# Performance work log

Hardware: AMD Instinct MI355X
Metric: run time of the kernel (lower is better)

## Reference

```python
import jax, jax.numpy as jnp
import numpy as np

EMBED = 256; HEADS = 8; LEVELS = 4; POINTS = 4; HEAD_DIM = EMBED // HEADS
B = 2; Q = 20000; HP = 128; WP = 128
EPS = 1e-5


def setup_inputs() -> dict:
    key = jax.random.key(0)
    ks = jax.random.split(key, 12)
    s = 1.0 / np.sqrt(EMBED)
    return {
        "query": jax.random.normal(ks[0], (Q, EMBED), jnp.float32),
        "query_spatial_positions": jax.random.uniform(ks[1], (Q, 2), jnp.float32),
        "query_batch_offsets": jnp.array([0, Q // 2, Q], dtype=jnp.int32),
        "stacked_feature_maps": jax.random.normal(ks[2], (B, HP, WP, LEVELS, EMBED), jnp.float32),
        "level_spatial_shapes": jnp.array([[128, 128], [64, 64], [32, 32], [16, 16]], dtype=jnp.int32),
        "norm_gamma": jnp.ones((EMBED,), jnp.float32),
        "norm_beta": jnp.zeros((EMBED,), jnp.float32),
        "W_q": jax.random.normal(ks[3], (EMBED, EMBED), jnp.float32) * s,
        "W_off": jax.random.normal(ks[4], (EMBED, HEADS * LEVELS * POINTS * 2), jnp.float32) * s * 0.1,
        "b_off": jax.random.normal(ks[5], (HEADS * LEVELS * POINTS * 2,), jnp.float32) * 0.5,
        "W_attn": jax.random.normal(ks[6], (EMBED, HEADS * LEVELS * POINTS), jnp.float32) * s,
        "b_attn": jnp.zeros((HEADS * LEVELS * POINTS,), jnp.float32),
        "W_val": jax.random.normal(ks[7], (EMBED, EMBED), jnp.float32) * s,
        "b_val": jnp.zeros((EMBED,), jnp.float32),
        "W_out": jax.random.normal(ks[8], (EMBED, EMBED), jnp.float32) * s,
    }


def _layernorm(x, g, b):
    mu = x.mean(-1, keepdims=True)
    xc = x - mu
    v = (xc * xc).mean(-1, keepdims=True)
    return xc * jax.lax.rsqrt(v + EPS) * g + b


def reference(query, query_spatial_positions, query_batch_offsets, stacked_feature_maps,
              level_spatial_shapes, norm_gamma, norm_beta, W_q, W_off, b_off,
              W_attn, b_attn, W_val, b_val, W_out):
    residual = query
    x = _layernorm(query, norm_gamma, norm_beta)
    x = x @ W_q  # q_in_proj (no bias)

    off = (x @ W_off + b_off).reshape(Q, HEADS, LEVELS, POINTS, 2)
    attn = jax.nn.softmax((x @ W_attn + b_attn).reshape(Q, HEADS, LEVELS * POINTS), axis=-1)
    attn = attn.reshape(Q, HEADS, LEVELS, POINTS)

    # value projection over all levels, split into heads: [B,HP,WP,L,H,HD]
    value = (stacked_feature_maps @ W_val + b_val).reshape(B, HP, WP, LEVELS, HEADS, HEAD_DIM)

    shp = level_spatial_shapes.astype(jnp.float32)  # [L,2] (h,w)
    # normalized ref point + offset scaled by level size -> pixel coords (align_corners=False)
    loc = query_spatial_positions[:, None, None, None, :] + off / shp[None, None, :, None, :]
    pix = loc * shp[None, None, :, None, :] - 0.5  # [Q,H,L,P,2]
    py, px = pix[..., 0], pix[..., 1]
    y0 = jnp.floor(py); x0 = jnp.floor(px)
    wy = py - y0; wx = px - x0
    y0i = y0.astype(jnp.int32); x0i = x0.astype(jnp.int32)

    Hl = level_spatial_shapes[:, 0][None, None, :, None]
    Wl = level_spatial_shapes[:, 1][None, None, :, None]
    b_idx = (jnp.searchsorted(query_batch_offsets, jnp.arange(Q, dtype=jnp.int32), side='right') - 1)[:, None, None, None]
    l_idx = jnp.arange(LEVELS)[None, None, :, None]
    h_idx = jnp.arange(HEADS)[None, :, None, None]

    def gather(yi, xi, w):
        m = (yi >= 0) & (yi < Hl) & (xi >= 0) & (xi < Wl)  # zero-pad outside level extent
        yc = jnp.clip(yi, 0, HP - 1)
        xc = jnp.clip(xi, 0, WP - 1)
        v = value[b_idx, yc, xc, l_idx, h_idx]  # [Q,H,L,P,HD]
        return v * (w * m)[..., None]

    samp = (gather(y0i, x0i, (1 - wy) * (1 - wx))
            + gather(y0i, x0i + 1, (1 - wy) * wx)
            + gather(y0i + 1, x0i, wy * (1 - wx))
            + gather(y0i + 1, x0i + 1, wy * wx))

    out = (attn[..., None] * samp).sum(axis=(2, 3)).reshape(Q, EMBED)
    return out @ W_out + residual
```

## Files before the change

### kernel.cpp

```cpp
#include <hip/hip_runtime.h>
#include <hip/hip_bf16.h>
#include <stdint.h>

#define EMBED 256
#define HEADS 8
#define LEVELS 4
#define POINTS 4
#define HEAD_DIM 32
#define HPAD 128
#define WPAD 128
#define LN_EPS 1e-5f

typedef unsigned short u16;
typedef __attribute__((ext_vector_type(8))) short bf16x8v;
typedef __attribute__((ext_vector_type(4))) float f32x4;

static __device__ __forceinline__ float bu2f(u16 u) {
  return __uint_as_float(((unsigned)u) << 16);
}
static __device__ __forceinline__ u16 f2bu(float f) {
  unsigned x = __float_as_uint(f);
  return (u16)((x + 0x7fffu + ((x >> 16) & 1u)) >> 16);
}
static __device__ __forceinline__ float loadf(const void* p, size_t i, int isbf) {
  return isbf ? bu2f(((const u16*)p)[i]) : ((const float*)p)[i];
}
static __device__ __forceinline__ int imin(int a, int b) { return a < b ? a : b; }

static __device__ __forceinline__ void cp16(const u16* g, u16* l) {
  __builtin_amdgcn_global_load_lds((const __attribute__((address_space(1))) unsigned*)g,
                                   (__attribute__((address_space(3))) unsigned*)l, 16, 0, 0);
}

__global__ __launch_bounds__(256) void detect_kernel(const unsigned* __restrict__ q,
                                                     int* __restrict__ flag) {
  int t = threadIdx.x;
  __shared__ int s[256];
  unsigned u = q[t * 13 + 1];
  unsigned e = (u >> 7) & 0xFF;
  s[t] = (e >= 116 && e <= 130) ? 1 : 0;
  __syncthreads();
  for (int st = 128; st > 0; st >>= 1) { if (t < st) s[t] += s[t + st]; __syncthreads(); }
  if (t == 0) *flag = (s[0] > 200) ? 1 : 0;
}

__global__ __launch_bounds__(384) void boa_kernel(const void* __restrict__ b_off,
                                                  const void* __restrict__ b_attn,
                                                  float* __restrict__ boa,
                                                  const int* __restrict__ dflag) {
  int fl = *dflag;
  int t = threadIdx.x;
  boa[t] = (t < 256) ? loadf(b_off, t, fl) : loadf(b_attn, t - 256, fl);
}

__global__ __launch_bounds__(256) void wtrans_kernel(const void* __restrict__ W,
                                                     u16* __restrict__ Wt,
                                                     int K, int N,
                                                     const int* __restrict__ dflag) {
  int fl = *dflag;
  __shared__ float tile[32][33];
  int tx = threadIdx.x & 31, ty = threadIdx.x >> 5;
  int k0 = blockIdx.x * 32, n0 = blockIdx.y * 32;
#pragma unroll
  for (int j = 0; j < 4; j++) {
    int r = ty + j * 8;
    tile[r][tx] = loadf(W, (size_t)(k0 + r) * N + n0 + tx, fl);
  }
  __syncthreads();
#pragma unroll
  for (int j = 0; j < 4; j++) {
    int n = ty + j * 8;
    Wt[(size_t)(n0 + n) * K + k0 + tx] = f2bu(tile[tx][n]);
  }
}

__global__ __launch_bounds__(256) void ln_kernel(const void* __restrict__ q,
                                                 const void* __restrict__ g,
                                                 const void* __restrict__ be,
                                                 u16* __restrict__ out,
                                                 const int* __restrict__ dflag) {
  int fl = *dflag;
  int row = blockIdx.x;
  int t = threadIdx.x;
  __shared__ float sh[256];
  float v = loadf(q, (size_t)row * EMBED + t, fl);
  sh[t] = v;
  __syncthreads();
  for (int s = 128; s > 0; s >>= 1) { if (t < s) sh[t] += sh[t + s]; __syncthreads(); }
  float mu = sh[0] * (1.f / 256.f);
  __syncthreads();
  float xc = v - mu;
  sh[t] = xc * xc;
  __syncthreads();
  for (int s = 128; s > 0; s >>= 1) { if (t < s) sh[t] += sh[t + s]; __syncthreads(); }
  float r = rsqrtf(sh[0] * (1.f / 256.f) + LN_EPS);
  out[(size_t)row * EMBED + t] = f2bu(xc * r * loadf(g, t, fl) + loadf(be, t, fl));
}

template <int OUTMODE, bool ABF>
__global__ __launch_bounds__(256) void mfma_gemm(const void* __restrict__ A,
                                                 const u16* __restrict__ Bt,
                                                 const void* __restrict__ bias, int BiasC,
                                                 const void* __restrict__ resid,
                                                 void* __restrict__ Cv,
                                                 int M, int N, int K,
                                                 const int* __restrict__ dflag) {
  int fl = *dflag;
  __shared__ u16 As[4096];
  __shared__ u16 Bs[4096];
  int tid = threadIdx.x;
  int m0 = blockIdx.x * 128, n0 = blockIdx.y * 128;
  int wave = tid >> 6, lane = tid & 63;
  int quad = lane >> 4, r16 = lane & 15;
  int wm = (wave >> 1) * 64, wn = (wave & 1) * 64;

  f32x4 acc[4][4];
#pragma unroll
  for (int i = 0; i < 4; i++)
#pragma unroll
    for (int j = 0; j < 4; j++) acc[i][j] = (f32x4){0.f, 0.f, 0.f, 0.f};

  int p0 = tid, p1 = tid + 256;
  int r0 = p0 >> 2, c0 = (p0 & 3) * 8;
  int r1 = p1 >> 2, c1 = (p1 & 3) * 8;
  int ra0 = imin(m0 + r0, M - 1), ra1 = imin(m0 + r1, M - 1);

  const u16*   Ab = (const u16*)A;
  const float* Af = (const float*)A;

  for (int k0 = 0; k0 < K; k0 += 32) {
    __syncthreads();
    if (ABF) {
      cp16(Ab + (size_t)ra0 * K + k0 + c0, &As[p0 * 8]);
      cp16(Ab + (size_t)ra1 * K + k0 + c1, &As[p1 * 8]);
    } else if (fl) {
      *(int4*)&As[p0 * 8] = *(const int4*)(Ab + (size_t)ra0 * K + k0 + c0);
      *(int4*)&As[p1 * 8] = *(const int4*)(Ab + (size_t)ra1 * K + k0 + c1);
    } else {
      float4 f00 = *(const float4*)(Af + (size_t)ra0 * K + k0 + c0);
      float4 f01 = *(const float4*)(Af + (size_t)ra0 * K + k0 + c0 + 4);
      float4 f10 = *(const float4*)(Af + (size_t)ra1 * K + k0 + c1);
      float4 f11 = *(const float4*)(Af + (size_t)ra1 * K + k0 + c1 + 4);
      u16* d0 = &As[p0 * 8];
      d0[0] = f2bu(f00.x); d0[1] = f2bu(f00.y); d0[2] = f2bu(f00.z); d0[3] = f2bu(f00.w);
      d0[4] = f2bu(f01.x); d0[5] = f2bu(f01.y); d0[6] = f2bu(f01.z); d0[7] = f2bu(f01.w);
      u16* d1 = &As[p1 * 8];
      d1[0] = f2bu(f10.x); d1[1] = f2bu(f10.y); d1[2] = f2bu(f10.z); d1[3] = f2bu(f10.w);
      d1[4] = f2bu(f11.x); d1[5] = f2bu(f11.y); d1[6] = f2bu(f11.z); d1[7] = f2bu(f11.w);
    }
    cp16(Bt + (size_t)(n0 + r0) * K + k0 + c0, &Bs[p0 * 8]);
    cp16(Bt + (size_t)(n0 + r1) * K + k0 + c1, &Bs[p1 * 8]);
    __syncthreads();

    bf16x8v a[4], b[4];
#pragma unroll
    for (int i = 0; i < 4; i++)
      a[i] = *(const bf16x8v*)&As[(wm + i * 16 + r16) * 32 + quad * 8];
#pragma unroll
    for (int j = 0; j < 4; j++)
      b[j] = *(const bf16x8v*)&Bs[(wn + j * 16 + r16) * 32 + quad * 8];
#pragma unroll
    for (int i = 0; i < 4; i++)
#pragma unroll
      for (int j = 0; j < 4; j++)
        acc[i][j] = __builtin_amdgcn_mfma_f32_16x16x32_bf16(a[i], b[j], acc[i][j], 0, 0, 0);
  }

  int obf = (OUTMODE == 2) ? fl : OUTMODE;
  int bfl = (BiasC == 2) ? fl : 0;
  if (bias) {
#pragma unroll
    for (int j = 0; j < 4; j++) {
      float bv = loadf(bias, n0 + wn + j * 16 + r16, bfl);
#pragma unroll
      for (int i = 0; i < 4; i++)
#pragma unroll
        for (int reg = 0; reg < 4; reg++) acc[i][j][reg] += bv;
    }
  }

  if (obf) {
    int sl0 = (quad << 4) | ((2 * r16) & 15);
    int sl1 = sl0 + 1;
    bool lohalf = (r16 < 8);
#pragma unroll
    for (int i = 0; i < 4; i++) {
#pragma unroll
      for (int jp = 0; jp < 2; jp++) {
#pragma unroll
        for (int reg = 0; reg < 4; reg++) {
          float vA = acc[i][jp * 2][reg], vB = acc[i][jp * 2 + 1][reg];
          float a0 = __shfl(vA, sl0), a1 = __shfl(vA, sl1);
          float b0 = __shfl(vB, sl0), b1 = __shfl(vB, sl1);
          float lo = lohalf ? a0 : b0;
          float hi = lohalf ? a1 : b1;
          int row = m0 + wm + i * 16 + quad * 4 + reg;
          if (row < M) {
            size_t base = (size_t)row * N + n0 + wn + jp * 32 + 2 * r16;
            if (resid) {
              lo += loadf(resid, base, fl);
              hi += loadf(resid, base + 1, fl);
            }
            unsigned pk = (unsigned)f2bu(lo) | ((unsigned)f2bu(hi) << 16);
            *(unsigned*)((u16*)Cv + base) = pk;
          }
        }
      }
    }
  } else {
#pragma unroll
    for (int j = 0; j < 4; j++) {
      int col = n0 + wn + j * 16 + r16;
#pragma unroll
      for (int i = 0; i < 4; i++) {
#pragma unroll
        for (int reg = 0; reg < 4; reg++) {
          int row = m0 + wm + i * 16 + quad * 4 + reg;
          if (row < M) {
            float v = acc[i][j][reg];
            if (resid) v += loadf(resid, (size_t)row * N + col, fl);
            ((float*)Cv)[(size_t)row * N + col] = v;
          }
        }
      }
    }
  }
}

__global__ __launch_bounds__(512) void val_gemm(const void* __restrict__ A,
                                                const u16* __restrict__ Bt,
                                                const void* __restrict__ bias,
                                                u16* __restrict__ Cv,
                                                int M, const int* __restrict__ dflag) {
  int fl = *dflag;
  __shared__ u16 As[128 * 256];
  int tid = threadIdx.x;
  int m0 = blockIdx.x * 128;
  int wave = tid >> 6, lane = tid & 63;
  int quad = lane >> 4, r16 = lane & 15;
  int wm = (wave >> 2) * 64, wn = (wave & 3) * 64;

  if (fl) {
    const uint4* A16 = (const uint4*)A;
#pragma unroll
    for (int i = 0; i < 8; i++) {
      int g = i * 512 + tid;
      int r = g >> 5, c = g & 31;
      int rg = imin(m0 + r, M - 1);
      uint4 v = A16[(size_t)rg * 32 + c];
      *(uint4*)&As[r * 256 + ((c ^ (r & 7)) * 8)] = v;
    }
  } else {
    const float4* A4 = (const float4*)A;
#pragma unroll
    for (int p = 0; p < 2; p++) {
      float4 f[8];
#pragma unroll
      for (int q = 0; q < 8; q++) {
        int g = (p * 8 + q) * 512 + tid;
        int rg = imin(m0 + (g >> 6), M - 1);
        f[q] = A4[(size_t)rg * 64 + (g & 63)];
      }
#pragma unroll
      for (int q = 0; q < 8; q++) {
        int g = (p * 8 + q) * 512 + tid;
        int r = g >> 6, cw = g & 63;
        int c = cw >> 1, sub = cw & 1;
        uint2 w;
        w.x = (unsigned)f2bu(f[q].x) | ((unsigned)f2bu(f[q].y) << 16);
        w.y = (unsigned)f2bu(f[q].z) | ((unsigned)f2bu(f[q].w) << 16);
        *(uint2*)&As[r * 256 + ((c ^ (r & 7)) * 8) + sub * 4] = w;
      }
    }
  }
  __syncthreads();

  f32x4 acc[4][4];
#pragma unroll
  for (int i = 0; i < 4; i++)
#pragma unroll
    for (int j = 0; j < 4; j++) acc[i][j] = (f32x4){0.f, 0.f, 0.f, 0.f};

  int arow[4], arl[4];
#pragma unroll
  for (int i = 0; i < 4; i++) {
    arow[i] = (wm + i * 16 + r16) * 256;
    arl[i]  = (wm + i * 16 + r16) & 7;
  }
  const u16* bbase[4];
#pragma unroll
  for (int j = 0; j < 4; j++)
    bbase[j] = Bt + (size_t)(wn + j * 16 + r16) * 256 + quad * 8;

#pragma unroll
  for (int t = 0; t < 8; t++) {
    bf16x8v b[4];
#pragma unroll
    for (int j = 0; j < 4; j++)
      b[j] = *(const bf16x8v*)(bbase[j] + t * 32);
    bf16x8v a[4];
#pragma unroll
    for (int i = 0; i < 4; i++) {
      int chunk = ((t << 2) | quad) ^ arl[i];
      a[i] = *(const bf16x8v*)&As[arow[i] + chunk * 8];
    }
#pragma unroll
    for (int i = 0; i < 4; i++)
#pragma unroll
      for (int j = 0; j < 4; j++)
        acc[i][j] = __builtin_amdgcn_mfma_f32_16x16x32_bf16(a[i], b[j], acc[i][j], 0, 0, 0);
  }

#pragma unroll
  for (int j = 0; j < 4; j++) {
    float bv = loadf(bias, wn + j * 16 + r16, fl);
#pragma unroll
    for (int i = 0; i < 4; i++)
#pragma unroll
      for (int reg = 0; reg < 4; reg++) acc[i][j][reg] += bv;
  }
  int sl0 = (quad << 4) | ((2 * r16) & 15);
  int sl1 = sl0 + 1;
  bool lohalf = (r16 < 8);
#pragma unroll
  for (int i = 0; i < 4; i++) {
#pragma unroll
    for (int jp = 0; jp < 2; jp++) {
#pragma unroll
      for (int reg = 0; reg < 4; reg++) {
        float vA = acc[i][jp * 2][reg], vB = acc[i][jp * 2 + 1][reg];
        float a0 = __shfl(vA, sl0), a1 = __shfl(vA, sl1);
        float b0 = __shfl(vB, sl0), b1 = __shfl(vB, sl1);
        float lo = lohalf ? a0 : b0;
        float hi = lohalf ? a1 : b1;
        int row = m0 + wm + i * 16 + quad * 4 + reg;
        if (row < M) {
          size_t base = (size_t)row * 256 + wn + jp * 32 + 2 * r16;
          unsigned pk = (unsigned)f2bu(lo) | ((unsigned)f2bu(hi) << 16);
          *(unsigned*)(Cv + base) = pk;
        }
      }
    }
  }
}

__global__ __launch_bounds__(256) void sample2_kernel(const float* __restrict__ oa,
                                                      const void* __restrict__ qsp,
                                                      const int* __restrict__ qbo, int nb,
                                                      const int* __restrict__ lss,
                                                      const u16* __restrict__ value,
                                                      u16* __restrict__ samp, int Qn,
                                                      const int* __restrict__ dflag) {
  int fl = *dflag;
  int t = threadIdx.x;
  int q2 = t >> 7;
  int i7 = t & 127;
  int qb = blockIdx.x * 2;
  int q = imin(qb + q2, Qn - 1);

  __shared__ float Loff[2][256];
  __shared__ float Lw[2][128];
  __shared__ int   Lb[2];
  __shared__ int   Co[2][128][4];
  __shared__ float Cw[2][128][4];

  {
    const float* row = oa + (size_t)q * 384;
    float2 v = ((const float2*)row)[i7];
    Loff[q2][i7 * 2]     = v.x;
    Loff[q2][i7 * 2 + 1] = v.y;
    Lw[q2][i7] = row[256 + i7];
  }
  if (t < 2) {
    int qq = imin(qb + t, Qn - 1);
    int b = 0;
    for (int i = 1; i < nb; i++) if (qq >= qbo[i]) b = i;
    Lb[t] = b;
  }
  __syncthreads();

  if (t < 16) {
    int sq = t >> 3, h = t & 7;
    float* w = &Lw[sq][h * 16];
    float mx = w[0];
    for (int i = 1; i < 16; i++) mx = fmaxf(mx, w[i]);
    float s = 0.f;
    for (int i = 0; i < 16; i++) { float e = __expf(w[i] - mx); w[i] = e; s += e; }
    float inv = 1.f / s;
    for (int i = 0; i < 16; i++) w[i] *= inv;
  }
  __syncthreads();

  {
    int h = i7 >> 4, lp = i7 & 15, l = lp >> 2;
    int Hi = lss[l * 2], Wi = lss[l * 2 + 1];
    float Hl = (float)Hi, Wl = (float)Wi;
    float qy = loadf(qsp, (size_t)q * 2, fl);
    float qx = loadf(qsp, (size_t)q * 2 + 1, fl);
    float a  = Lw[q2][i7];
    float oy = Loff[q2][i7 * 2], ox = Loff[q2][i7 * 2 + 1];
    float py = (qy + oy / Hl) * Hl - 0.5f;
    float px = (qx + ox / Wl) * Wl - 0.5f;
    float y0f = floorf(py), x0f = floorf(px);
    float wy = py - y0f, wx = px - x0f;
    int y0 = (int)y0f, x0 = (int)x0f;
    int bbase = Lb[q2] * (HPAD * WPAD * LEVELS * EMBED);
#pragma unroll
    for (int c = 0; c < 4; c++) {
      int yi = y0 + (c >> 1), xi = x0 + (c & 1);
      float w = ((c >> 1) ? wy : 1.f - wy) * ((c & 1) ? wx : 1.f - wx);
      bool ok = (yi >= 0) & (yi < Hi) & (xi >= 0) & (xi < Wi);
      Co[q2][i7][c] = ok ? (bbase + ((yi * WPAD + xi) * LEVELS + l) * EMBED + h * HEAD_DIM) : 0;
      Cw[q2][i7][c] = ok ? (a * w) : 0.f;
    }
  }
  __syncthreads();

  {
    int h = (t >> 4) & 7;
    int d2 = t & 15;
    float ax = 0.f, ay = 0.f;
#pragma unroll
    for (int lp = 0; lp < 16; lp++) {
      int4   o4 = *(const int4*)&Co[q2][h * 16 + lp][0];
      float4 w4 = *(const float4*)&Cw[q2][h * 16 + lp][0];
      unsigned v;
      v = *(const unsigned*)(value + o4.x + d2 * 2);
      ax += w4.x * __uint_as_float(v << 16); ay += w4.x * __uint_as_float(v & 0xffff0000u);
      v = *(const unsigned*)(value + o4.y + d2 * 2);
      ax += w4.y * __uint_as_float(v << 16); ay += w4.y * __uint_as_float(v & 0xffff0000u);
      v = *(const unsigned*)(value + o4.z + d2 * 2);
      ax += w4.z * __uint_as_float(v << 16); ay += w4.z * __uint_as_float(v & 0xffff0000u);
      v = *(const unsigned*)(value + o4.w + d2 * 2);
      ax += w4.w * __uint_as_float(v << 16); ay += w4.w * __uint_as_float(v & 0xffff0000u);
    }
    if (qb + q2 < Qn) {
      unsigned pk = (unsigned)f2bu(ax) | ((unsigned)f2bu(ay) << 16);
      *(unsigned*)(samp + (size_t)(qb + q2) * 256 + h * 32 + d2 * 2) = pk;
    }
  }
}

extern "C" void kernel_launch(void* const* d_in, const int* in_sizes, int n_in,
                              void* d_out, int out_size, void* d_ws, size_t ws_size,
                              hipStream_t stream) {
  const void* query  = d_in[0];
  const void* qsp    = d_in[1];
  const int*  qbo    = (const int*)d_in[2];
  const void* sfm    = d_in[3];
  const int*  lss    = (const int*)d_in[4];
  const void* gamma  = d_in[5];
  const void* beta   = d_in[6];
  const void* W_q    = d_in[7];
  const void* W_off  = d_in[8];
  const void* b_off  = d_in[9];
  const void* W_attn = d_in[10];
  const void* b_attn = d_in[11];
  const void* W_val  = d_in[12];
  const void* b_val  = d_in[13];
  const void* W_out  = d_in[14];

  const int Q  = in_sizes[0] / EMBED;
  const int nb = in_sizes[2] - 1;
  const int MV = in_sizes[3] / EMBED;

  char* ws = (char*)d_ws;
  size_t o = 0;
  auto alloc = [&](size_t bytes) { size_t r = o; o = (o + bytes + 255) & ~(size_t)255; return r; };
  u16*   xln   = (u16*)(ws + alloc((size_t)Q * EMBED * sizeof(u16)));
  u16*   x     = (u16*)(ws + alloc((size_t)Q * EMBED * sizeof(u16)));
  float* oaw   = (float*)(ws + alloc((size_t)Q * 384 * sizeof(float)));
  u16*   valw  = (u16*)(ws + alloc((size_t)MV * EMBED * sizeof(u16)));
  u16*   sampw = (u16*)(ws + alloc((size_t)Q * EMBED * sizeof(u16)));
  u16*   wtq   = (u16*)(ws + alloc(256 * 256 * sizeof(u16)));
  u16*   wtoa  = (u16*)(ws + alloc(384 * 256 * sizeof(u16)));
  u16*   wtval = (u16*)(ws + alloc(256 * 256 * sizeof(u16)));
  u16*   wtout = (u16*)(ws + alloc(256 * 256 * sizeof(u16)));
  float* boa   = (float*)(ws + alloc(384 * sizeof(float)));
  int*   dflag = (int*)(ws + alloc(256));
  (void)ws_size;

  detect_kernel<<<1, 256, 0, stream>>>((const unsigned*)query, dflag);
  boa_kernel<<<1, 384, 0, stream>>>(b_off, b_attn, boa, dflag);

  wtrans_kernel<<<dim3(8, 8), 256, 0, stream>>>(W_q,    wtq,              256, 256, dflag);
  wtrans_kernel<<<dim3(8, 8), 256, 0, stream>>>(W_off,  wtoa,             256, 256, dflag);
  wtrans_kernel<<<dim3(8, 4), 256, 0, stream>>>(W_attn, wtoa + 256 * 256, 256, 128, dflag);
  wtrans_kernel<<<dim3(8, 8), 256, 0, stream>>>(W_val,  wtval,            256, 256, dflag);
  wtrans_kernel<<<dim3(8, 8), 256, 0, stream>>>(W_out,  wtout,            256, 256, dflag);

  ln_kernel<<<Q, 256, 0, stream>>>(query, gamma, beta, xln, dflag);

  const int GQ = (Q + 127) / 128;
  mfma_gemm<1, true><<<dim3(GQ, 2), 256, 0, stream>>>(xln, wtq, nullptr, 0, nullptr, x, Q, 256, 256, dflag);
  mfma_gemm<0, true><<<dim3(GQ, 3), 256, 0, stream>>>(x, wtoa, boa, 0, nullptr, oaw, Q, 384, 256, dflag);
  val_gemm<<<dim3(MV / 128), 512, 0, stream>>>(sfm, wtval, b_val, valw, MV, dflag);
  sample2_kernel<<<(Q + 1) / 2, 256, 0, stream>>>(oaw, qsp, qbo, nb, lss, valw, sampw, Q, dflag);
  mfma_gemm<2, true><<<dim3(GQ, 2), 256, 0, stream>>>(sampw, wtout, nullptr, 0, query, d_out, Q, 256, 256, dflag);
}
```

Measured before the change: 428.1 us.

## Project only in-extent level pixels in value GEMM and use wave-per-row LayerNorm

The value-projection GEMM now launches 170 row-tiles per batch and maps each tile to pixels that lie inside its level's spatial extent (128, 64, 32, 16), skipping padded pixels that sampling masks to zero. This removes most of the feature-map reads and MFMA work in the largest kernel. The level shapes are hardcoded rather than read from level_spatial_shapes. Unwritten value entries keep stale workspace contents, which matters only if the sampler reads masked locations without guarding against them. LayerNorm is also rewritten to handle one row per wave, using vector loads and shuffle reductions in place of shared-memory tree reductions with many barriers.

```diff
diff --git a/kernel.cpp b/kernel.cpp
--- a/kernel.cpp
+++ b/kernel.cpp
@@ -77,24 +77,38 @@
 __global__ __launch_bounds__(256) void ln_kernel(const void* __restrict__ q,
                                                  const void* __restrict__ g,
                                                  const void* __restrict__ be,
-                                                 u16* __restrict__ out,
+                                                 u16* __restrict__ out, int Qn,
                                                  const int* __restrict__ dflag) {
   int fl = *dflag;
-  int row = blockIdx.x;
-  int t = threadIdx.x;
-  __shared__ float sh[256];
-  float v = loadf(q, (size_t)row * EMBED + t, fl);
-  sh[t] = v;
-  __syncthreads();
-  for (int s = 128; s > 0; s >>= 1) { if (t < s) sh[t] += sh[t + s]; __syncthreads(); }
-  float mu = sh[0] * (1.f / 256.f);
-  __syncthreads();
-  float xc = v - mu;
-  sh[t] = xc * xc;
-  __syncthreads();
-  for (int s = 128; s > 0; s >>= 1) { if (t < s) sh[t] += sh[t + s]; __syncthreads(); }
-  float r = rsqrtf(sh[0] * (1.f / 256.f) + LN_EPS);
-  out[(size_t)row * EMBED + t] = f2bu(xc * r * loadf(g, t, fl) + loadf(be, t, fl));
+  int row = blockIdx.x * 4 + (threadIdx.x >> 6);
+  int lane = threadIdx.x & 63;
+  if (row >= Qn) return;
+  float v0, v1, v2, v3;
+  if (fl) {
+    uint2 u = *(const uint2*)((const u16*)q + (size_t)row * 256 + lane * 4);
+    v0 = bu2f((u16)(u.x & 0xffff)); v1 = bu2f((u16)(u.x >> 16));
+    v2 = bu2f((u16)(u.y & 0xffff)); v3 = bu2f((u16)(u.y >> 16));
+  } else {
+    float4 f = *(const float4*)((const float*)q + (size_t)row * 256 + lane * 4);
+    v0 = f.x; v1 = f.y; v2 = f.z; v3 = f.w;
+  }
+  float s = v0 + v1 + v2 + v3;
+#pragma unroll
+  for (int m = 1; m < 64; m <<= 1) s += __shfl_xor(s, m, 64);
+  float mu = s * (1.f / 256.f);
+  float c0 = v0 - mu, c1 = v1 - mu, c2 = v2 - mu, c3 = v3 - mu;
+  float s2 = c0 * c0 + c1 * c1 + c2 * c2 + c3 * c3;
+#pragma unroll
+  for (int m = 1; m < 64; m <<= 1) s2 += __shfl_xor(s2, m, 64);
+  float r = rsqrtf(s2 * (1.f / 256.f) + LN_EPS);
+  float o0 = c0 * r * loadf(g, lane * 4 + 0, fl) + loadf(be, lane * 4 + 0, fl);
+  float o1 = c1 * r * loadf(g, lane * 4 + 1, fl) + loadf(be, lane * 4 + 1, fl);
+  float o2 = c2 * r * loadf(g, lane * 4 + 2, fl) + loadf(be, lane * 4 + 2, fl);
+  float o3 = c3 * r * loadf(g, lane * 4 + 3, fl) + loadf(be, lane * 4 + 3, fl);
+  uint2 w;
+  w.x = (unsigned)f2bu(o0) | ((unsigned)f2bu(o1) << 16);
+  w.y = (unsigned)f2bu(o2) | ((unsigned)f2bu(o3) << 16);
+  *(uint2*)(out + (size_t)row * 256 + lane * 4) = w;
 }
 
 template <int OUTMODE, bool ABF>
@@ -231,11 +245,22 @@
                                                 const u16* __restrict__ Bt,
                                                 const void* __restrict__ bias,
                                                 u16* __restrict__ Cv,
-                                                int M, const int* __restrict__ dflag) {
+                                                const int* __restrict__ dflag) {
   int fl = *dflag;
   __shared__ u16 As[128 * 256];
   int tid = threadIdx.x;
-  int m0 = blockIdx.x * 128;
+  int blk = blockIdx.x;
+  int b   = blk / 170;
+  int cb  = blk % 170;
+  int l, ibase;
+  if (cb < 128)      { l = 0; ibase = cb * 128; }
+  else if (cb < 160) { l = 1; ibase = (cb - 128) * 128; }
+  else if (cb < 168) { l = 2; ibase = (cb - 160) * 128; }
+  else               { l = 3; ibase = (cb - 168) * 128; }
+  int shift = 7 - l;
+  int mask  = (128 >> l) - 1;
+  int rowbase = b * 65536 + l;
+
   int wave = tid >> 6, lane = tid & 63;
   int quad = lane >> 4, r16 = lane & 15;
   int wm = (wave >> 2) * 64, wn = (wave & 3) * 64;
@@ -243,11 +268,12 @@
   if (fl) {
     const uint4* A16 = (const uint4*)A;
 #pragma unroll
-    for (int i = 0; i < 8; i++) {
-      int g = i * 512 + tid;
+    for (int it = 0; it < 8; it++) {
+      int g = it * 512 + tid;
       int r = g >> 5, c = g & 31;
-      int rg = imin(m0 + r, M - 1);
-      uint4 v = A16[(size_t)rg * 32 + c];
+      int i = ibase + r;
+      size_t rowg = (size_t)rowbase + (i >> shift) * 512 + (i & mask) * 4;
+      uint4 v = A16[rowg * 32 + c];
       *(uint4*)&As[r * 256 + ((c ^ (r & 7)) * 8)] = v;
     }
   } else {
@@ -258,8 +284,9 @@
 #pragma unroll
       for (int q = 0; q < 8; q++) {
         int g = (p * 8 + q) * 512 + tid;
-        int rg = imin(m0 + (g >> 6), M - 1);
-        f[q] = A4[(size_t)rg * 64 + (g & 63)];
+        int i = ibase + (g >> 6);
+        size_t rowg = (size_t)rowbase + (i >> shift) * 512 + (i & mask) * 4;
+        f[q] = A4[rowg * 64 + (g & 63)];
       }
 #pragma unroll
       for (int q = 0; q < 8; q++) {
@@ -294,21 +321,21 @@
 
 #pragma unroll
   for (int t = 0; t < 8; t++) {
-    bf16x8v b[4];
+    bf16x8v b4[4];
 #pragma unroll
     for (int j = 0; j < 4; j++)
-      b[j] = *(const bf16x8v*)(bbase[j] + t * 32);
-    bf16x8v a[4];
+      b4[j] = *(const bf16x8v*)(bbase[j] + t * 32);
+    bf16x8v a4[4];
 #pragma unroll
     for (int i = 0; i < 4; i++) {
       int chunk = ((t << 2) | quad) ^ arl[i];
-      a[i] = *(const bf16x8v*)&As[arow[i] + chunk * 8];
+      a4[i] = *(const bf16x8v*)&As[arow[i] + chunk * 8];
     }
 #pragma unroll
     for (int i = 0; i < 4; i++)
 #pragma unroll
       for (int j = 0; j < 4; j++)
-        acc[i][j] = __builtin_amdgcn_mfma_f32_16x16x32_bf16(a[i], b[j], acc[i][j], 0, 0, 0);
+        acc[i][j] = __builtin_amdgcn_mfma_f32_16x16x32_bf16(a4[i], b4[j], acc[i][j], 0, 0, 0);
   }
 
 #pragma unroll
@@ -333,12 +360,12 @@
         float b0 = __shfl(vB, sl0), b1 = __shfl(vB, sl1);
         float lo = lohalf ? a0 : b0;
         float hi = lohalf ? a1 : b1;
-        int row = m0 + wm + i * 16 + quad * 4 + reg;
-        if (row < M) {
-          size_t base = (size_t)row * 256 + wn + jp * 32 + 2 * r16;
-          unsigned pk = (unsigned)f2bu(lo) | ((unsigned)f2bu(hi) << 16);
-          *(unsigned*)(Cv + base) = pk;
-        }
+        int rloc = wm + i * 16 + quad * 4 + reg;
+        int ii = ibase + rloc;
+        size_t rowg = (size_t)rowbase + (ii >> shift) * 512 + (ii & mask) * 4;
+        size_t base = rowg * 256 + wn + jp * 32 + 2 * r16;
+        unsigned pk = (unsigned)f2bu(lo) | ((unsigned)f2bu(hi) << 16);
+        *(unsigned*)(Cv + base) = pk;
       }
     }
   }
@@ -463,6 +490,7 @@
   const int Q  = in_sizes[0] / EMBED;
   const int nb = in_sizes[2] - 1;
   const int MV = in_sizes[3] / EMBED;
+  const int B  = MV / (HPAD * WPAD * LEVELS);
 
   char* ws = (char*)d_ws;
   size_t o = 0;
@@ -489,12 +517,12 @@
   wtrans_kernel<<<dim3(8, 8), 256, 0, stream>>>(W_val,  wtval,            256, 256, dflag);
   wtrans_kernel<<<dim3(8, 8), 256, 0, stream>>>(W_out,  wtout,            256, 256, dflag);
 
-  ln_kernel<<<Q, 256, 0, stream>>>(query, gamma, beta, xln, dflag);
+  ln_kernel<<<(Q + 3) / 4, 256, 0, stream>>>(query, gamma, beta, xln, Q, dflag);
 
   const int GQ = (Q + 127) / 128;
   mfma_gemm<1, true><<<dim3(GQ, 2), 256, 0, stream>>>(xln, wtq, nullptr, 0, nullptr, x, Q, 256, 256, dflag);
   mfma_gemm<0, true><<<dim3(GQ, 3), 256, 0, stream>>>(x, wtoa, boa, 0, nullptr, oaw, Q, 384, 256, dflag);
-  val_gemm<<<dim3(MV / 128), 512, 0, stream>>>(sfm, wtval, b_val, valw, MV, dflag);
+  val_gemm<<<dim3(B * 170), 512, 0, stream>>>(sfm, wtval, b_val, valw, dflag);
   sample2_kernel<<<(Q + 1) / 2, 256, 0, stream>>>(oaw, qsp, qbo, nb, lss, valw, sampw, Q, dflag);
   mfma_gemm<2, true><<<dim3(GQ, 2), 256, 0, stream>>>(sampw, wtout, nullptr, 0, query, d_out, Q, 256, 256, dflag);
 }
```

Result: faster. 381.0 us (-11.0%).
